# Kernel optimization log

Hardware: AMD Instinct MI355X
Metric: run time of the kernel (lower is better)

Reference implementation:

```python
import jax, jax.numpy as jnp
import numpy as np

B, T, Y, X, E, TR, R = 64, 1024, 512, 128, 512, 512, 512


def setup_inputs() -> dict:
    key = jax.random.key(0)
    ks = iter(jax.random.split(key, 48))

    def w(shape, s=0.05):
        return (jax.random.normal(next(ks), shape, jnp.float32) * s)

    z = lambda *s: jnp.zeros(s, jnp.float32)
    inp = dict(
        data=jax.random.uniform(next(ks), (B, T, Y), jnp.float32),
        eps_q=jax.random.normal(next(ks), (T, B, X), jnp.float32),
        eps_p=jax.random.normal(next(ks), (T, B, X), jnp.float32),
        # RNN (single layer, relu nonlinearity)
        rnn_Wih=w((Y, R)), rnn_Whh=w((R, R)), rnn_bih=z(R), rnn_bhh=z(R),
        h0=z(R), xq0=z(X), x0=z(X),
        # GaussianCombiner
        comb_Wxh=w((X, R)), comb_bxh=z(R),
        comb_Whm=w((R, X)), comb_bhm=z(X),
        comb_Whl=w((R, X)), comb_bhl=z(X),
        # GaussianGatedTransition
        t_Wg1=w((X, TR)), t_bg1=z(TR), t_Wg2=w((TR, X)), t_bg2=z(X),
        t_Wp1=w((X, TR)), t_bp1=z(TR), t_Wp2=w((TR, X)), t_bp2=z(X),
        t_Wmu=jnp.eye(X, dtype=jnp.float32), t_bmu=z(X),  # torch inits lin_x_to_mu to identity
        t_Wlv=w((X, X)), t_blv=z(X),
        # BernoulliEmitter
        e_W1=w((X, E)), e_b1=z(E), e_W2=w((E, E)), e_b2=z(E),
        e_W3=w((E, Y)), e_b3=z(Y),
    )
    return inp


def reference(data, eps_q, eps_p,
              rnn_Wih, rnn_Whh, rnn_bih, rnn_bhh, h0, xq0, x0,
              comb_Wxh, comb_bxh, comb_Whm, comb_bhm, comb_Whl, comb_bhl,
              t_Wg1, t_bg1, t_Wg2, t_bg2, t_Wp1, t_bp1, t_Wp2, t_bp2,
              t_Wmu, t_bmu, t_Wlv, t_blv,
              e_W1, e_b1, e_W2, e_b2, e_W3, e_b3):
    Bx = data.shape[0]

    # ---- inference RNN: run on time-reversed data, then reverse output back ----
    # precompute input projection for all steps: [T, B, R]
    x_proj = (jnp.einsum('bty,yr->btr', data[:, ::-1, :], rnn_Wih)
              + rnn_bih + rnn_bhh).transpose(1, 0, 2)

    def rnn_step(h, xp):
        h = jax.nn.relu(xp + h @ rnn_Whh)
        return h, h

    h_init = jnp.broadcast_to(h0, (Bx, R))
    _, hs = jax.lax.scan(rnn_step, h_init, x_proj)  # [T, B, R]
    rnn_out = hs[::-1]  # back to original time order, aligned with data

    # ---- inference network: sequential combiner + reparameterize ----
    def inf_step(x_prev, inputs):
        h_rnn, eps = inputs
        h_c = 0.5 * (jnp.tanh(x_prev @ comb_Wxh + comb_bxh) + h_rnn)
        mu = h_c @ comb_Whm + comb_bhm
        lv = h_c @ comb_Whl + comb_bhl
        x_t = mu + eps * jnp.exp(0.5 * lv)
        return x_t, (x_t, mu, lv)

    xq0b = jnp.broadcast_to(xq0, (Bx, X))
    _, (q_x, q_mu, q_lv) = jax.lax.scan(inf_step, xq0b, (rnn_out, eps_q))
    q_x, q_mu, q_lv = (a.transpose(1, 0, 2) for a in (q_x, q_mu, q_lv))  # [B,T,X]

    # ---- generative model: sequential gated transition ----
    def gen_step(x_prev, eps):
        gate = jax.nn.sigmoid(jax.nn.relu(x_prev @ t_Wg1 + t_bg1) @ t_Wg2 + t_bg2)
        pm = jax.nn.relu(x_prev @ t_Wp1 + t_bp1) @ t_Wp2 + t_bp2
        mu = (1.0 - gate) * (x_prev @ t_Wmu + t_bmu) + gate * pm
        lv = jax.nn.relu(pm) @ t_Wlv + t_blv
        x_t = mu + eps * jnp.exp(0.5 * lv)
        return x_t, (x_t, mu, lv)

    x0b = jnp.broadcast_to(x0, (Bx, X))
    _, (p_x, p_mu, p_lv) = jax.lax.scan(gen_step, x0b, eps_p)
    p_x, p_mu, p_lv = (a.transpose(1, 0, 2) for a in (p_x, p_mu, p_lv))  # [B,T,X]

    # ---- emitter over all (b, t) at once ----
    h1 = jax.nn.relu(jnp.einsum('btx,xe->bte', q_x, e_W1) + e_b1)
    h2 = jax.nn.relu(jnp.einsum('bte,ef->btf', h1, e_W2) + e_b2)
    y_probs = jax.nn.sigmoid(jnp.einsum('bte,ey->bty', h2, e_W3) + e_b3)

    return (q_x, q_mu, q_lv, p_x, p_mu, p_lv, y_probs)
```

## Files before the change

kernel.cpp:

```cpp
#include <hip/hip_runtime.h>
#include <stdint.h>

typedef __bf16 bf16x8 __attribute__((ext_vector_type(8)));
typedef short  s16x8  __attribute__((ext_vector_type(8)));
typedef float  f32x4  __attribute__((ext_vector_type(4)));

#define MFMA16(a, b, c) __builtin_amdgcn_mfma_f32_16x16x32_bf16((a), (b), (c), 0, 0, 0)

#define OFF_X      0ull
#define OFF_QXBF   67108864ull
#define OFF_WIH    83886080ull
#define OFF_WHH    84410368ull
#define OFF_WXH    84934656ull
#define OFF_WICAT  85065728ull
#define OFF_W1CAT  85327872ull
#define OFF_WG2    85590016ull
#define OFF_WP2    85721088ull
#define OFF_WMU    85852160ull
#define OFF_WLV    85884928ull
#define OFF_EW1    85917696ull
#define OFF_EW2    86048768ull
#define OFF_EW3    86573056ull
#define OFF_B1CAT  87097344ull
#define OFF_BICAT  87101440ull
#define OFF_XPCNT  87364608ull

#define QX_O  0ull
#define QMU_O 8388608ull
#define QLV_O 16777216ull
#define PX_O  25165824ull
#define PMU_O 33554432ull
#define PLV_O 41943040ull
#define Y_O   50331648ull

#define SMEM_SCAN 131072
#define SMEM_EMIS 133120

struct P {
  char* ws; float* out;
  const float *data, *eps_q, *eps_p;
  const float *Wih, *Whh, *bih, *bhh, *h0, *xq0, *x0;
  const float *Wxh, *bxh, *Whm, *bhm, *Whl, *bhl;
  const float *Wg1, *bg1, *Wg2, *bg2, *Wp1, *bp1, *Wp2, *bp2, *Wmu, *bmu, *Wlv, *blv;
  const float *eW1, *eb1, *eW2, *eb2, *eW3, *eb3;
};

__device__ __forceinline__ short f2bf(float f) {
  union { float f; uint32_t u; } v; v.f = f;
  uint32_t r = (v.u + 0x7FFFu + ((v.u >> 16) & 1u)) >> 16;
  return (short)(uint16_t)r;
}
__device__ __forceinline__ float bf2f(short s) {
  union { uint32_t u; float f; } v; v.u = ((uint32_t)(uint16_t)s) << 16;
  return v.f;
}
__device__ __forceinline__ bf16x8 ldfrag(const short* pp) { return *(const bf16x8*)pp; }
__device__ __forceinline__ bf16x8 cvt8p(const float* pp) {
  bf16x8 r;
#pragma unroll
  for (int i = 0; i < 8; ++i) r[i] = (__bf16)pp[i];
  return r;
}
__device__ __forceinline__ bf16x8 relu8(bf16x8 a) {
  s16x8 s = __builtin_bit_cast(s16x8, a);
#pragma unroll
  for (int i = 0; i < 8; ++i) s[i] = (s[i] < 0) ? (short)0 : s[i];
  return __builtin_bit_cast(bf16x8, s);
}

__device__ __forceinline__ void relfence() {
  asm volatile("s_waitcnt vmcnt(0)" ::: "memory");
}
__device__ __forceinline__ void st_sc16(short* pp, short v) {
  __hip_atomic_store(pp, v, __ATOMIC_RELAXED, __HIP_MEMORY_SCOPE_AGENT);
}
__device__ __forceinline__ short ld_sc16(const short* pp) {
  return __hip_atomic_load((short*)pp, __ATOMIC_RELAXED, __HIP_MEMORY_SCOPE_AGENT);
}
__device__ __forceinline__ int ldflag(int* pp) {
  return __hip_atomic_load(pp, __ATOMIC_RELAXED, __HIP_MEMORY_SCOPE_AGENT);
}
__device__ __forceinline__ void barrier_lgkm() {
  __builtin_amdgcn_sched_barrier(0);
  asm volatile("s_waitcnt lgkmcnt(0)" ::: "memory");
  __builtin_amdgcn_s_barrier();
  __builtin_amdgcn_sched_barrier(0);
}

__device__ __forceinline__ void pack_w(short* dst, const float* src, int KT, int N, int idx) {
  int tile = idx >> 9, rem = idx & 511;
  int lane = rem >> 3, j = rem & 7;
  int nt = tile / KT, kt = tile - nt * KT;
  int k = kt * 32 + ((lane >> 4) << 3) + j, n = (nt << 4) + (lane & 15);
  dst[idx] = f2bf(src[(int64_t)k * N + n]);
}

__global__ void __launch_bounds__(256) k_prep(P p) {
  char* ws = p.ws;
  const int64_t total = 1608032;
  for (int64_t i = (int64_t)blockIdx.x * 256 + threadIdx.x; i < total;
       i += (int64_t)gridDim.x * 256) {
    int64_t r = i;
    if (r < 262144) { pack_w((short*)(ws + OFF_WIH), p.Wih, 16, 512, (int)r); continue; }
    r -= 262144;
    if (r < 262144) { pack_w((short*)(ws + OFF_WHH), p.Whh, 16, 512, (int)r); continue; }
    r -= 262144;
    if (r < 65536) { pack_w((short*)(ws + OFF_WXH), p.Wxh, 4, 512, (int)r); continue; }
    r -= 65536;
    if (r < 131072) {
      int idx = (int)r;
      int tile = idx >> 9, rem = idx & 511, lane = rem >> 3, jj = rem & 7;
      int nt = tile >> 4, kt = tile & 15;
      int k = kt * 32 + ((lane >> 4) << 3) + jj, ccol = (nt << 4) + (lane & 15);
      int pair = ccol >> 7, within = ccol & 127, sub = within >> 6;
      int col = (within & 63) + (pair << 6);
      const float* s = sub ? p.Whl : p.Whm;
      ((short*)(ws + OFF_WICAT))[idx] = f2bf(s[(int64_t)k * 128 + col]);
      continue;
    }
    r -= 131072;
    if (r < 131072) {
      int idx = (int)r;
      int tile = idx >> 9, rem = idx & 511, lane = rem >> 3, jj = rem & 7;
      int nt = tile >> 2, kt = tile & 3;
      int k = kt * 32 + ((lane >> 4) << 3) + jj, ccol = (nt << 4) + (lane & 15);
      const float* s = (ccol < 512) ? p.Wg1 : p.Wp1;
      ((short*)(ws + OFF_W1CAT))[idx] = f2bf(s[(int64_t)k * 512 + (ccol & 511)]);
      continue;
    }
    r -= 131072;
    if (r < 65536) { pack_w((short*)(ws + OFF_WG2), p.Wg2, 16, 128, (int)r); continue; }
    r -= 65536;
    if (r < 65536) { pack_w((short*)(ws + OFF_WP2), p.Wp2, 16, 128, (int)r); continue; }
    r -= 65536;
    if (r < 16384) { pack_w((short*)(ws + OFF_WMU), p.Wmu, 4, 128, (int)r); continue; }
    r -= 16384;
    if (r < 16384) { pack_w((short*)(ws + OFF_WLV), p.Wlv, 4, 128, (int)r); continue; }
    r -= 16384;
    if (r < 65536) { pack_w((short*)(ws + OFF_EW1), p.eW1, 4, 512, (int)r); continue; }
    r -= 65536;
    if (r < 262144) { pack_w((short*)(ws + OFF_EW2), p.eW2, 16, 512, (int)r); continue; }
    r -= 262144;
    if (r < 262144) { pack_w((short*)(ws + OFF_EW3), p.eW3, 16, 512, (int)r); continue; }
    r -= 262144;
    if (r < 1024) { ((float*)(ws + OFF_B1CAT))[r] = (r < 512) ? p.bg1[r] : p.bp1[r - 512]; continue; }
    r -= 1024;
    if (r < 256) {
      int ccol = (int)r; int pair = ccol >> 7, within = ccol & 127, sub = within >> 6;
      int col = (within & 63) + (pair << 6);
      ((float*)(ws + OFF_BICAT))[ccol] = sub ? p.bhl[col] : p.bhm[col];
      continue;
    }
    r -= 256;
    ((int*)(ws + OFF_XPCNT))[r] = 0;
  }
}

__global__ void __launch_bounds__(512, 2) k_scan(P p) {
  extern __shared__ char smem[];
  char* ws = p.ws;
  const int tid = threadIdx.x;
  const int lane = tid & 63, w = tid >> 6;
  const int l16 = lane & 15, quad = lane >> 4;
  const int wg = blockIdx.x;

  short* Xb   = (short*)(ws + OFF_X);
  short* qxbf = (short*)(ws + OFF_QXBF);
  int* xp_cnt = (int*)(ws + OFF_XPCNT);

  if (wg < 64) {
    const int s = wg & 7, t0 = wg >> 3;
    const int mrow4 = (w & 3) * 16;
    const int nt0 = s * 4 + (w >> 2) * 2;
    const short* wih = (const short*)(ws + OFF_WIH);
    for (int tt = 0; tt < 128; ++tt) {
      const int t = t0 + (tt << 3);
      const int tsrc = 1023 - t;
      const float* arow = p.data + ((size_t)(mrow4 + l16) * 1024 + tsrc) * 512 + quad * 8;
      f32x4 acc[2] = {};
      for (int kt = 0; kt < 16; ++kt) {
        bf16x8 af = cvt8p(arow + kt * 32);
#pragma unroll
        for (int i = 0; i < 2; ++i) {
          bf16x8 bw = ldfrag(wih + ((size_t)((nt0 + i) * 16 + kt) * 64 + lane) * 8);
          acc[i] = MFMA16(af, bw, acc[i]);
        }
      }
      short* xrow = Xb + (size_t)t * 32768;
#pragma unroll
      for (int i = 0; i < 2; ++i) {
        const int col = (nt0 + i) * 16 + l16;
        const float bias = p.bih[col] + p.bhh[col];
#pragma unroll
        for (int r = 0; r < 4; ++r) {
          const int row = mrow4 + quad * 4 + r;
          st_sc16(xrow + (size_t)row * 512 + col, f2bf(acc[i][r] + bias));
        }
      }
      relfence();
      __syncthreads();
      if (tid == 0) atomicAdd(xp_cnt + t, 1);
    }
    return;
  }

  if (wg < 68) {
    const int g = wg - 64;
    short* whh_l = (short*)smem;
    char* hbuf = smem + 98304;
    {
      const float4* src4 = (const float4*)(ws + OFF_WHH);
      float4* dst4 = (float4*)smem;
      for (int i2 = tid; i2 < 6144; i2 += 512) {
        const int blk = i2 >> 6, wi = i2 & 63;
        const int nt = blk / 3, kk = blk - nt * 3;
        dst4[(size_t)blk * 64 + wi] = src4[(size_t)(nt * 16 + 13 + kk) * 64 + wi];
      }
    }
    const short* whh = (const short*)(ws + OFF_WHH);
    bf16x8 wb[4][13];
#pragma unroll
    for (int i = 0; i < 4; ++i) {
      const int nt = w * 4 + i;
#pragma unroll
      for (int kt = 0; kt < 13; ++kt)
        wb[i][kt] = ldfrag(whh + ((size_t)(nt * 16 + kt) * 64 + lane) * 8);
    }
    __syncthreads();
    while (ldflag(xp_cnt) < 8) __builtin_amdgcn_s_sleep(2);
    short xv[4][4];
#pragma unroll
    for (int i = 0; i < 4; ++i) {
      const int col = (w * 4 + i) * 16 + l16;
#pragma unroll
      for (int r = 0; r < 4; ++r)
        xv[i][r] = ld_sc16(Xb + (size_t)(g * 16 + quad * 4 + r) * 512 + col);
    }
    {
      f32x4 acc[4] = {};
#pragma unroll
      for (int c = 0; c < 8; ++c) {
        bf16x8 a2[2];
#pragma unroll
        for (int k2 = 0; k2 < 2; ++k2) a2[k2] = cvt8p(p.h0 + (c * 2 + k2) * 32 + quad * 8);
#pragma unroll
        for (int k2 = 0; k2 < 2; ++k2) {
          const int kt = c * 2 + k2;
#pragma unroll
          for (int i = 0; i < 4; ++i) {
            bf16x8 bw = (kt < 13)
                ? wb[i][kt]
                : ldfrag(whh_l + ((size_t)((w * 4 + i) * 3 + (kt - 13)) * 64 + lane) * 8);
            acc[i] = MFMA16(a2[k2], bw, acc[i]);
          }
        }
      }
      char* hw = hbuf;
      short* xrow = Xb;
#pragma unroll
      for (int i = 0; i < 4; ++i) {
        const int col = (w * 4 + i) * 16 + l16;
#pragma unroll
        for (int r = 0; r < 4; ++r) {
          const int row = quad * 4 + r;
          float h = acc[i][r] + bf2f(xv[i][r]);
          const short hv = f2bf(h > 0.f ? h : 0.f);
          *(short*)(hw + row * 1024 + ((col * 2) ^ ((row & 7) << 4))) = hv;
          st_sc16(xrow + (size_t)(g * 16 + row) * 512 + col, hv);
        }
      }
      while (ldflag(xp_cnt + 1) < 8) __builtin_amdgcn_s_sleep(2);
      const short* xn = Xb + 32768;
#pragma unroll
      for (int i = 0; i < 4; ++i) {
        const int col = (w * 4 + i) * 16 + l16;
#pragma unroll
        for (int r = 0; r < 4; ++r)
          xv[i][r] = ld_sc16(xn + (size_t)(g * 16 + quad * 4 + r) * 512 + col);
      }
      barrier_lgkm();
    }
    for (int t = 1; t < 1024; ++t) {
      const char* hb = hbuf + ((t - 1) & 1) * 16384;
      f32x4 acc[4] = {};
#pragma unroll
      for (int c = 0; c < 8; ++c) {
        bf16x8 a2[2];
#pragma unroll
        for (int k2 = 0; k2 < 2; ++k2) {
          const int kt = c * 2 + k2;
          a2[k2] = ldfrag((const short*)(hb + l16 * 1024 +
                     ((kt * 64 + quad * 16) ^ ((l16 & 7) << 4))));
        }
#pragma unroll
        for (int k2 = 0; k2 < 2; ++k2) {
          const int kt = c * 2 + k2;
#pragma unroll
          for (int i = 0; i < 4; ++i) {
            bf16x8 bw = (kt < 13)
                ? wb[i][kt]
                : ldfrag(whh_l + ((size_t)((w * 4 + i) * 3 + (kt - 13)) * 64 + lane) * 8);
            acc[i] = MFMA16(a2[k2], bw, acc[i]);
          }
        }
      }
      char* hw = hbuf + (t & 1) * 16384;
      short* xrow = Xb + (size_t)t * 32768;
#pragma unroll
      for (int i = 0; i < 4; ++i) {
        const int col = (w * 4 + i) * 16 + l16;
#pragma unroll
        for (int r = 0; r < 4; ++r) {
          const int row = quad * 4 + r;
          float h = acc[i][r] + bf2f(xv[i][r]);
          const short hv = f2bf(h > 0.f ? h : 0.f);
          *(short*)(hw + row * 1024 + ((col * 2) ^ ((row & 7) << 4))) = hv;
          st_sc16(xrow + (size_t)(g * 16 + row) * 512 + col, hv);
        }
      }
      if (t < 1023) {
        int* fc = xp_cnt + t + 1;
        while (ldflag(fc) < 8) __builtin_amdgcn_s_sleep(2);
        const short* xn = Xb + (size_t)(t + 1) * 32768;
#pragma unroll
        for (int i = 0; i < 4; ++i) {
          const int col = (w * 4 + i) * 16 + l16;
#pragma unroll
          for (int r = 0; r < 4; ++r)
            xv[i][r] = ld_sc16(xn + (size_t)(g * 16 + quad * 4 + r) * 512 + col);
        }
      }
      barrier_lgkm();
    }
    relfence();
    __syncthreads();
    const int g2 = g;
    char* hcs = smem;
    char* xqs = smem + 16384;
    float* scr = (float*)(smem + 20480);
    const short* wxh = (const short*)(ws + OFF_WXH);
    const short* wicat = (const short*)(ws + OFF_WICAT);
    const float* bicat = (const float*)(ws + OFF_BICAT);
    bf16x8 wa[4][4];
    float bx[4];
#pragma unroll
    for (int i = 0; i < 4; ++i) {
      const int nt = w * 4 + i;
#pragma unroll
      for (int kt = 0; kt < 4; ++kt)
        wa[i][kt] = ldfrag(wxh + ((size_t)(nt * 4 + kt) * 64 + lane) * 8);
      bx[i] = p.bxh[nt * 16 + l16];
    }
    bf16x8 wbv[2][16];
    float bias2[2];
#pragma unroll
    for (int i = 0; i < 2; ++i) {
      const int nt = w * 2 + i;
#pragma unroll
      for (int kt = 0; kt < 16; ++kt)
        wbv[i][kt] = ldfrag(wicat + ((size_t)(nt * 16 + kt) * 64 + lane) * 8);
      bias2[i] = bicat[nt * 16 + l16];
    }
    for (int t = 0; t < 1024; ++t) {
      short rv[4][4];
      const short* rsrc = Xb + (size_t)(1023 - t) * 32768;
#pragma unroll
      for (int i = 0; i < 4; ++i) {
        const int ng = (w * 4 + i) * 16 + l16;
#pragma unroll
        for (int r = 0; r < 4; ++r)
          rv[i][r] = ld_sc16(rsrc + (size_t)(g2 * 16 + quad * 4 + r) * 512 + ng);
      }
      float ev[4];
#pragma unroll
      for (int q2 = 0; q2 < 4; ++q2) {
        const int idx = tid + q2 * 512;
        const int row = idx >> 7, cl = idx & 127;
        ev[q2] = p.eps_q[((size_t)t * 64 + g2 * 16 + row) * 128 + cl];
      }
      bf16x8 af1[4];
      if (t == 0) {
#pragma unroll
        for (int kt = 0; kt < 4; ++kt) af1[kt] = cvt8p(p.xq0 + kt * 32 + quad * 8);
      } else {
#pragma unroll
        for (int kt = 0; kt < 4; ++kt)
          af1[kt] = ldfrag((const short*)(xqs + l16 * 256 +
                     ((kt * 64 + quad * 16) ^ ((l16 & 7) << 4))));
      }
      f32x4 acc1[4] = {};
#pragma unroll
      for (int kt = 0; kt < 4; ++kt)
#pragma unroll
        for (int i = 0; i < 4; ++i) acc1[i] = MFMA16(af1[kt], wa[i][kt], acc1[i]);
#pragma unroll
      for (int i = 0; i < 4; ++i) {
        const int ng = (w * 4 + i) * 16 + l16;
#pragma unroll
        for (int r = 0; r < 4; ++r) {
          const int row = quad * 4 + r;
          const float u = acc1[i][r] + bx[i];
          const float e = __expf(2.f * u);
          const float th = 1.f - 2.f / (e + 1.f);
          const float hcv = 0.5f * (th + bf2f(rv[i][r]));
          *(short*)(hcs + row * 1024 + ((ng * 2) ^ ((row & 7) << 4))) = f2bf(hcv);
        }
      }
      barrier_lgkm();
      f32x4 acc2[2] = {};
#pragma unroll
      for (int c = 0; c < 4; ++c) {
        bf16x8 a4[4];
#pragma unroll
        for (int k2 = 0; k2 < 4; ++k2) {
          const int kt = c * 4 + k2;
          a4[k2] = ldfrag((const short*)(hcs + l16 * 1024 +
                     ((kt * 64 + quad * 16) ^ ((l16 & 7) << 4))));
        }
#pragma unroll
        for (int k2 = 0; k2 < 4; ++k2)
#pragma unroll
          for (int i = 0; i < 2; ++i) acc2[i] = MFMA16(a4[k2], wbv[i][c * 4 + k2], acc2[i]);
      }
#pragma unroll
      for (int i = 0; i < 2; ++i) {
        const int catcol = (w * 2 + i) * 16 + l16;
        const int within = catcol & 127, sub = within >> 6;
        const int col = (within & 63) + ((catcol >> 7) << 6);
        float* dbase = p.out + (sub ? QLV_O : QMU_O);
#pragma unroll
        for (int r = 0; r < 4; ++r) {
          const int row = quad * 4 + r;
          const float v = acc2[i][r] + bias2[i];
          dbase[(size_t)(g2 * 16 + row) * 131072 + (size_t)t * 128 + col] = v;
          scr[(sub * 16 + row) * 128 + col] = v;
        }
      }
      barrier_lgkm();
#pragma unroll
      for (int q2 = 0; q2 < 4; ++q2) {
        const int idx = tid + q2 * 512;
        const int row = idx >> 7, cl = idx & 127;
        const int b = g2 * 16 + row;
        const float m = scr[row * 128 + cl], l = scr[(16 + row) * 128 + cl];
        const float xvv = m + ev[q2] * __expf(0.5f * l);
        p.out[QX_O + (size_t)b * 131072 + (size_t)t * 128 + cl] = xvv;
        const short xb = f2bf(xvv);
        qxbf[((size_t)b * 1024 + t) * 128 + cl] = xb;
        *(short*)(xqs + row * 256 + ((cl * 2) ^ ((row & 7) << 4))) = xb;
      }
      barrier_lgkm();
    }
    return;
  }

  {
    const int g3 = wg - 68;
    short* ldsWmu = (short*)smem;
    short* ldsWlv = (short*)(smem + 32768);
    char* xls  = smem + 65536;
    char* u1ls = smem + 69632;
    char* pmls = smem + 102400;
    {
      const float4* s1 = (const float4*)(ws + OFF_WMU);
      const float4* s2 = (const float4*)(ws + OFF_WLV);
      float4* d1 = (float4*)smem;
      float4* d2 = (float4*)(smem + 32768);
      for (int i2 = tid; i2 < 2048; i2 += 512) { d1[i2] = s1[i2]; d2[i2] = s2[i2]; }
    }
    const short* w1cat = (const short*)(ws + OFF_W1CAT);
    const float* b1cat = (const float*)(ws + OFF_B1CAT);
    const short* wp2g = (const short*)(ws + OFF_WP2);
    const short* wg2g = (const short*)(ws + OFF_WG2);
    bf16x8 w1[8][4];
    float b1[8];
#pragma unroll
    for (int i = 0; i < 8; ++i) {
      const int nt = w * 8 + i;
#pragma unroll
      for (int kt = 0; kt < 4; ++kt)
        w1[i][kt] = ldfrag(w1cat + ((size_t)(nt * 4 + kt) * 64 + lane) * 8);
      b1[i] = b1cat[nt * 16 + l16];
    }
    const int colw = w * 16 + l16;
    const float bpv = p.bp2[colw], bgv = p.bg2[colw], bmv = p.bmu[colw], blvv = p.blv[colw];
    __syncthreads();
    for (int t = 0; t < 1024; ++t) {
      float ep[4];
#pragma unroll
      for (int r = 0; r < 4; ++r)
        ep[r] = p.eps_p[((size_t)t * 64 + g3 * 16 + quad * 4 + r) * 128 + colw];
      bf16x8 ax[4];
      if (t == 0) {
#pragma unroll
        for (int kt = 0; kt < 4; ++kt) ax[kt] = cvt8p(p.x0 + kt * 32 + quad * 8);
      } else {
#pragma unroll
        for (int kt = 0; kt < 4; ++kt)
          ax[kt] = ldfrag((const short*)(xls + l16 * 256 +
                     ((kt * 64 + quad * 16) ^ ((l16 & 7) << 4))));
      }
#pragma unroll
      for (int hf = 0; hf < 2; ++hf) {
        f32x4 a1[4] = {};
#pragma unroll
        for (int kt = 0; kt < 4; ++kt)
#pragma unroll
          for (int i = 0; i < 4; ++i) a1[i] = MFMA16(ax[kt], w1[hf * 4 + i][kt], a1[i]);
#pragma unroll
        for (int i = 0; i < 4; ++i) {
          const int c1 = (w * 8 + hf * 4 + i) * 16 + l16;
#pragma unroll
          for (int r = 0; r < 4; ++r) {
            const int row = quad * 4 + r;
            const float u = a1[i][r] + b1[hf * 4 + i];
            *(short*)(u1ls + row * 2048 + ((c1 * 2) ^ ((row & 7) << 4))) = f2bf(u > 0.f ? u : 0.f);
          }
        }
      }
      barrier_lgkm();
      f32x4 apm = {}, ag = {}, axm = {};
#pragma unroll
      for (int c = 0; c < 8; ++c) {
        bf16x8 bpf[2], bgf[2];
#pragma unroll
        for (int k2 = 0; k2 < 2; ++k2) {
          bpf[k2] = ldfrag(wp2g + ((size_t)(w * 16 + c * 2 + k2) * 64 + lane) * 8);
          bgf[k2] = ldfrag(wg2g + ((size_t)(w * 16 + c * 2 + k2) * 64 + lane) * 8);
        }
        bf16x8 aup[2], aug[2];
#pragma unroll
        for (int k2 = 0; k2 < 2; ++k2) {
          const int kt = c * 2 + k2;
          aup[k2] = ldfrag((const short*)(u1ls + l16 * 2048 +
                      ((1024 + kt * 64 + quad * 16) ^ ((l16 & 7) << 4))));
          aug[k2] = ldfrag((const short*)(u1ls + l16 * 2048 +
                      ((kt * 64 + quad * 16) ^ ((l16 & 7) << 4))));
        }
#pragma unroll
        for (int k2 = 0; k2 < 2; ++k2) {
          apm = MFMA16(aup[k2], bpf[k2], apm);
          ag  = MFMA16(aug[k2], bgf[k2], ag);
        }
      }
#pragma unroll
      for (int kt = 0; kt < 4; ++kt) {
        bf16x8 bw = ldfrag(ldsWmu + ((size_t)(w * 4 + kt) * 64 + lane) * 8);
        axm = MFMA16(ax[kt], bw, axm);
      }
      float pmv[4];
#pragma unroll
      for (int r = 0; r < 4; ++r) {
        const int row = quad * 4 + r;
        pmv[r] = apm[r] + bpv;
        *(short*)(pmls + row * 256 + ((colw * 2) ^ ((row & 7) << 4))) = f2bf(pmv[r]);
      }
      barrier_lgkm();
      bf16x8 apf[4];
#pragma unroll
      for (int kt = 0; kt < 4; ++kt)
        apf[kt] = relu8(ldfrag((const short*)(pmls + l16 * 256 +
                    ((kt * 64 + quad * 16) ^ ((l16 & 7) << 4)))));
      f32x4 alv = {};
#pragma unroll
      for (int kt = 0; kt < 4; ++kt) {
        bf16x8 bw = ldfrag(ldsWlv + ((size_t)(w * 4 + kt) * 64 + lane) * 8);
        alv = MFMA16(apf[kt], bw, alv);
      }
#pragma unroll
      for (int r = 0; r < 4; ++r) {
        const int row = quad * 4 + r, b = g3 * 16 + row;
        const float lv = alv[r] + blvv;
        const float gv = 1.f / (1.f + __expf(-(ag[r] + bgv)));
        const float xmv = axm[r] + bmv;
        const float mu = (1.f - gv) * xmv + gv * pmv[r];
        const float xvv = mu + ep[r] * __expf(0.5f * lv);
        *(short*)(xls + row * 256 + ((colw * 2) ^ ((row & 7) << 4))) = f2bf(xvv);
        p.out[PMU_O + (size_t)b * 131072 + (size_t)t * 128 + colw] = mu;
        p.out[PLV_O + (size_t)b * 131072 + (size_t)t * 128 + colw] = lv;
        p.out[PX_O  + (size_t)b * 131072 + (size_t)t * 128 + colw] = xvv;
      }
      barrier_lgkm();
    }
    return;
  }
}

__global__ void __launch_bounds__(256) k_emis(P p) {
  extern __shared__ char smem[];
  short* h1 = (short*)smem;
  short* h2 = (short*)(smem + 66560);
  const int tid = threadIdx.x, lane = tid & 63, w = tid >> 6;
  const int l16 = lane & 15, quad = lane >> 4;
  const size_t m0 = (size_t)blockIdx.x * 64;
  const short* qx  = (const short*)(p.ws + OFF_QXBF);
  const short* ew1 = (const short*)(p.ws + OFF_EW1);
  const short* ew2 = (const short*)(p.ws + OFF_EW2);
  const short* ew3 = (const short*)(p.ws + OFF_EW3);
  for (int nc = 0; nc < 2; ++nc) {
    f32x4 acc[4][4] = {};
    for (int kt = 0; kt < 4; ++kt) {
      bf16x8 bw[4];
#pragma unroll
      for (int i = 0; i < 4; ++i) {
        const int nt = w * 8 + nc * 4 + i;
        bw[i] = ldfrag(ew1 + ((size_t)(nt * 4 + kt) * 64 + lane) * 8);
      }
#pragma unroll
      for (int mt = 0; mt < 4; ++mt) {
        bf16x8 af = ldfrag(qx + (m0 + mt * 16 + l16) * 128 + kt * 32 + quad * 8);
#pragma unroll
        for (int i = 0; i < 4; ++i) acc[mt][i] = MFMA16(af, bw[i], acc[mt][i]);
      }
    }
#pragma unroll
    for (int mt = 0; mt < 4; ++mt)
#pragma unroll
      for (int i = 0; i < 4; ++i) {
        const int col = (w * 8 + nc * 4 + i) * 16 + l16;
        const float bias = p.eb1[col];
#pragma unroll
        for (int r = 0; r < 4; ++r) {
          const float v = acc[mt][i][r] + bias;
          h1[(mt * 16 + quad * 4 + r) * 520 + col] = f2bf(v > 0.f ? v : 0.f);
        }
      }
  }
  __syncthreads();
  for (int nc = 0; nc < 2; ++nc) {
    f32x4 acc[4][4] = {};
    for (int kt = 0; kt < 16; ++kt) {
      bf16x8 bw[4];
#pragma unroll
      for (int i = 0; i < 4; ++i) {
        const int nt = w * 8 + nc * 4 + i;
        bw[i] = ldfrag(ew2 + ((size_t)(nt * 16 + kt) * 64 + lane) * 8);
      }
#pragma unroll
      for (int mt = 0; mt < 4; ++mt) {
        bf16x8 af = ldfrag(h1 + (mt * 16 + l16) * 520 + kt * 32 + quad * 8);
#pragma unroll
        for (int i = 0; i < 4; ++i) acc[mt][i] = MFMA16(af, bw[i], acc[mt][i]);
      }
    }
#pragma unroll
    for (int mt = 0; mt < 4; ++mt)
#pragma unroll
      for (int i = 0; i < 4; ++i) {
        const int col = (w * 8 + nc * 4 + i) * 16 + l16;
        const float bias = p.eb2[col];
#pragma unroll
        for (int r = 0; r < 4; ++r) {
          const float v = acc[mt][i][r] + bias;
          h2[(mt * 16 + quad * 4 + r) * 520 + col] = f2bf(v > 0.f ? v : 0.f);
        }
      }
  }
  __syncthreads();
  for (int nc = 0; nc < 2; ++nc) {
    f32x4 acc[4][4] = {};
    for (int kt = 0; kt < 16; ++kt) {
      bf16x8 bw[4];
#pragma unroll
      for (int i = 0; i < 4; ++i) {
        const int nt = w * 8 + nc * 4 + i;
        bw[i] = ldfrag(ew3 + ((size_t)(nt * 16 + kt) * 64 + lane) * 8);
      }
#pragma unroll
      for (int mt = 0; mt < 4; ++mt) {
        bf16x8 af = ldfrag(h2 + (mt * 16 + l16) * 520 + kt * 32 + quad * 8);
#pragma unroll
        for (int i = 0; i < 4; ++i) acc[mt][i] = MFMA16(af, bw[i], acc[mt][i]);
      }
    }
#pragma unroll
    for (int mt = 0; mt < 4; ++mt)
#pragma unroll
      for (int i = 0; i < 4; ++i) {
        const int col = (w * 8 + nc * 4 + i) * 16 + l16;
        const float bias = p.eb3[col];
#pragma unroll
        for (int r = 0; r < 4; ++r) {
          const size_t m = m0 + mt * 16 + quad * 4 + r;
          const size_t b = m >> 10, tt2 = m & 1023;
          const float v = acc[mt][i][r] + bias;
          p.out[Y_O + (b << 19) + tt2 * 512 + col] = 1.f / (1.f + __expf(-v));
        }
      }
  }
}

extern "C" void kernel_launch(void* const* d_in, const int* in_sizes, int n_in,
                              void* d_out, int out_size, void* d_ws, size_t ws_size,
                              hipStream_t stream) {
  (void)in_sizes; (void)n_in; (void)out_size; (void)ws_size;
  P p;
  p.ws = (char*)d_ws; p.out = (float*)d_out;
  p.data = (const float*)d_in[0];
  p.eps_q = (const float*)d_in[1];
  p.eps_p = (const float*)d_in[2];
  p.Wih = (const float*)d_in[3]; p.Whh = (const float*)d_in[4];
  p.bih = (const float*)d_in[5]; p.bhh = (const float*)d_in[6];
  p.h0 = (const float*)d_in[7]; p.xq0 = (const float*)d_in[8]; p.x0 = (const float*)d_in[9];
  p.Wxh = (const float*)d_in[10]; p.bxh = (const float*)d_in[11];
  p.Whm = (const float*)d_in[12]; p.bhm = (const float*)d_in[13];
  p.Whl = (const float*)d_in[14]; p.bhl = (const float*)d_in[15];
  p.Wg1 = (const float*)d_in[16]; p.bg1 = (const float*)d_in[17];
  p.Wg2 = (const float*)d_in[18]; p.bg2 = (const float*)d_in[19];
  p.Wp1 = (const float*)d_in[20]; p.bp1 = (const float*)d_in[21];
  p.Wp2 = (const float*)d_in[22]; p.bp2 = (const float*)d_in[23];
  p.Wmu = (const float*)d_in[24]; p.bmu = (const float*)d_in[25];
  p.Wlv = (const float*)d_in[26]; p.blv = (const float*)d_in[27];
  p.eW1 = (const float*)d_in[28]; p.eb1 = (const float*)d_in[29];
  p.eW2 = (const float*)d_in[30]; p.eb2 = (const float*)d_in[31];
  p.eW3 = (const float*)d_in[32]; p.eb3 = (const float*)d_in[33];

  hipFuncSetAttribute(reinterpret_cast<const void*>(k_scan),
                      hipFuncAttributeMaxDynamicSharedMemorySize, SMEM_SCAN);
  hipFuncSetAttribute(reinterpret_cast<const void*>(k_emis),
                      hipFuncAttributeMaxDynamicSharedMemorySize, SMEM_EMIS);

  k_prep<<<dim3(2048), dim3(256), 0, stream>>>(p);
  k_scan<<<dim3(72), dim3(512), SMEM_SCAN, stream>>>(p);
  k_emis<<<dim3(1024), dim3(256), SMEM_EMIS, stream>>>(p);
}
```

Measured before the change: 12.99 ms.

## Split input projection into its own kernel and drop per-step flag polling

The input projection (data @ Wih) moves out of the persistent scan kernel into a separate 512-block kernel that runs before the scan. The scan grid shrinks from 72 to 8 workgroups. This removes the per-timestep counter flags, the spin-wait polling and the agent-scope atomic 16-bit loads and stores on the RNN critical path; plain loads and stores replace them. In exchange, the projection no longer overlaps with the recurrence and adds a serialized launch. Any remaining cross-workgroup handoff of RNN outputs now uses plain loads, which may rely on coherence guarantees the code does not enforce.

```diff
diff --git a/kernel.cpp b/kernel.cpp
--- a/kernel.cpp
+++ b/kernel.cpp
@@ -23,7 +23,6 @@
 #define OFF_EW3    86573056ull
 #define OFF_B1CAT  87097344ull
 #define OFF_BICAT  87101440ull
-#define OFF_XPCNT  87364608ull
 
 #define QX_O  0ull
 #define QMU_O 8388608ull
@@ -67,18 +66,8 @@
   for (int i = 0; i < 8; ++i) s[i] = (s[i] < 0) ? (short)0 : s[i];
   return __builtin_bit_cast(bf16x8, s);
 }
-
 __device__ __forceinline__ void relfence() {
   asm volatile("s_waitcnt vmcnt(0)" ::: "memory");
-}
-__device__ __forceinline__ void st_sc16(short* pp, short v) {
-  __hip_atomic_store(pp, v, __ATOMIC_RELAXED, __HIP_MEMORY_SCOPE_AGENT);
-}
-__device__ __forceinline__ short ld_sc16(const short* pp) {
-  return __hip_atomic_load((short*)pp, __ATOMIC_RELAXED, __HIP_MEMORY_SCOPE_AGENT);
-}
-__device__ __forceinline__ int ldflag(int* pp) {
-  return __hip_atomic_load(pp, __ATOMIC_RELAXED, __HIP_MEMORY_SCOPE_AGENT);
 }
 __device__ __forceinline__ void barrier_lgkm() {
   __builtin_amdgcn_sched_barrier(0);
@@ -97,7 +86,7 @@
 
 __global__ void __launch_bounds__(256) k_prep(P p) {
   char* ws = p.ws;
-  const int64_t total = 1608032;
+  const int64_t total = 1606912;
   for (int64_t i = (int64_t)blockIdx.x * 256 + threadIdx.x; i < total;
        i += (int64_t)gridDim.x * 256) {
     int64_t r = i;
@@ -151,12 +140,47 @@
       ((float*)(ws + OFF_BICAT))[ccol] = sub ? p.bhl[col] : p.bhm[col];
       continue;
     }
-    r -= 256;
-    ((int*)(ws + OFF_XPCNT))[r] = 0;
   }
 }
 
-__global__ void __launch_bounds__(512, 2) k_scan(P p) {
+__global__ void __launch_bounds__(256) k_xproj(P p) {
+  char* ws = p.ws;
+  const int tid = threadIdx.x;
+  const int lane = tid & 63, w = tid >> 6;
+  const int l16 = lane & 15, quad = lane >> 4;
+  const int s = blockIdx.x & 7, t0 = blockIdx.x >> 3;
+  short* Xb = (short*)(ws + OFF_X);
+  const short* wih = (const short*)(ws + OFF_WIH);
+  for (int tt = 0; tt < 16; ++tt) {
+    const int t = t0 + (tt << 6);
+    const int tsrc = 1023 - t;
+    const float* arow = p.data + ((size_t)(w * 16 + l16) * 1024 + tsrc) * 512 + quad * 8;
+    f32x4 acc[4] = {};
+    for (int kt = 0; kt < 16; ++kt) {
+      bf16x8 af = cvt8p(arow + kt * 32);
+#pragma unroll
+      for (int i = 0; i < 4; ++i) {
+        const int nt = s * 4 + i;
+        bf16x8 bw = ldfrag(wih + ((size_t)(nt * 16 + kt) * 64 + lane) * 8);
+        acc[i] = MFMA16(af, bw, acc[i]);
+      }
+    }
+    short* xrow = Xb + (size_t)t * 32768;
+#pragma unroll
+    for (int i = 0; i < 4; ++i) {
+      const int col = (s * 4 + i) * 16 + l16;
+      const float bias = p.bih[col] + p.bhh[col];
+#pragma unroll
+      for (int r = 0; r < 4; ++r) {
+        const int row = w * 16 + quad * 4 + r;
+        xrow[(size_t)row * 512 + col] = f2bf(acc[i][r] + bias);
+      }
+    }
+  }
+}
+
+__global__ void __launch_bounds__(512)
+__attribute__((amdgpu_waves_per_eu(2, 2))) k_scan(P p) {
   extern __shared__ char smem[];
   char* ws = p.ws;
   const int tid = threadIdx.x;
@@ -166,46 +190,9 @@
 
   short* Xb   = (short*)(ws + OFF_X);
   short* qxbf = (short*)(ws + OFF_QXBF);
-  int* xp_cnt = (int*)(ws + OFF_XPCNT);
-
-  if (wg < 64) {
-    const int s = wg & 7, t0 = wg >> 3;
-    const int mrow4 = (w & 3) * 16;
-    const int nt0 = s * 4 + (w >> 2) * 2;
-    const short* wih = (const short*)(ws + OFF_WIH);
-    for (int tt = 0; tt < 128; ++tt) {
-      const int t = t0 + (tt << 3);
-      const int tsrc = 1023 - t;
-      const float* arow = p.data + ((size_t)(mrow4 + l16) * 1024 + tsrc) * 512 + quad * 8;
-      f32x4 acc[2] = {};
-      for (int kt = 0; kt < 16; ++kt) {
-        bf16x8 af = cvt8p(arow + kt * 32);
-#pragma unroll
-        for (int i = 0; i < 2; ++i) {
-          bf16x8 bw = ldfrag(wih + ((size_t)((nt0 + i) * 16 + kt) * 64 + lane) * 8);
-          acc[i] = MFMA16(af, bw, acc[i]);
-        }
-      }
-      short* xrow = Xb + (size_t)t * 32768;
-#pragma unroll
-      for (int i = 0; i < 2; ++i) {
-        const int col = (nt0 + i) * 16 + l16;
-        const float bias = p.bih[col] + p.bhh[col];
-#pragma unroll
-        for (int r = 0; r < 4; ++r) {
-          const int row = mrow4 + quad * 4 + r;
-          st_sc16(xrow + (size_t)row * 512 + col, f2bf(acc[i][r] + bias));
-        }
-      }
-      relfence();
-      __syncthreads();
-      if (tid == 0) atomicAdd(xp_cnt + t, 1);
-    }
-    return;
-  }
-
-  if (wg < 68) {
-    const int g = wg - 64;
+
+  if (wg < 4) {
+    const int g = wg;
     short* whh_l = (short*)smem;
     char* hbuf = smem + 98304;
     {
@@ -227,14 +214,13 @@
         wb[i][kt] = ldfrag(whh + ((size_t)(nt * 16 + kt) * 64 + lane) * 8);
     }
     __syncthreads();
-    while (ldflag(xp_cnt) < 8) __builtin_amdgcn_s_sleep(2);
     short xv[4][4];
 #pragma unroll
     for (int i = 0; i < 4; ++i) {
       const int col = (w * 4 + i) * 16 + l16;
 #pragma unroll
       for (int r = 0; r < 4; ++r)
-        xv[i][r] = ld_sc16(Xb + (size_t)(g * 16 + quad * 4 + r) * 512 + col);
+        xv[i][r] = Xb[(size_t)(g * 16 + quad * 4 + r) * 512 + col];
     }
     {
       f32x4 acc[4] = {};
@@ -256,7 +242,6 @@
         }
       }
       char* hw = hbuf;
-      short* xrow = Xb;
 #pragma unroll
       for (int i = 0; i < 4; ++i) {
         const int col = (w * 4 + i) * 16 + l16;
@@ -266,17 +251,16 @@
           float h = acc[i][r] + bf2f(xv[i][r]);
           const short hv = f2bf(h > 0.f ? h : 0.f);
           *(short*)(hw + row * 1024 + ((col * 2) ^ ((row & 7) << 4))) = hv;
-          st_sc16(xrow + (size_t)(g * 16 + row) * 512 + col, hv);
-        }
-      }
-      while (ldflag(xp_cnt + 1) < 8) __builtin_amdgcn_s_sleep(2);
+          Xb[(size_t)(g * 16 + row) * 512 + col] = hv;
+        }
+      }
       const short* xn = Xb + 32768;
 #pragma unroll
       for (int i = 0; i < 4; ++i) {
         const int col = (w * 4 + i) * 16 + l16;
 #pragma unroll
         for (int r = 0; r < 4; ++r)
-          xv[i][r] = ld_sc16(xn + (size_t)(g * 16 + quad * 4 + r) * 512 + col);
+          xv[i][r] = xn[(size_t)(g * 16 + quad * 4 + r) * 512 + col];
       }
       barrier_lgkm();
     }
@@ -315,19 +299,17 @@
           float h = acc[i][r] + bf2f(xv[i][r]);
           const short hv = f2bf(h > 0.f ? h : 0.f);
           *(short*)(hw + row * 1024 + ((col * 2) ^ ((row & 7) << 4))) = hv;
-          st_sc16(xrow + (size_t)(g * 16 + row) * 512 + col, hv);
+          xrow[(size_t)(g * 16 + row) * 512 + col] = hv;
         }
       }
       if (t < 1023) {
-        int* fc = xp_cnt + t + 1;
-        while (ldflag(fc) < 8) __builtin_amdgcn_s_sleep(2);
         const short* xn = Xb + (size_t)(t + 1) * 32768;
 #pragma unroll
         for (int i = 0; i < 4; ++i) {
           const int col = (w * 4 + i) * 16 + l16;
 #pragma unroll
           for (int r = 0; r < 4; ++r)
-            xv[i][r] = ld_sc16(xn + (size_t)(g * 16 + quad * 4 + r) * 512 + col);
+            xv[i][r] = xn[(size_t)(g * 16 + quad * 4 + r) * 512 + col];
         }
       }
       barrier_lgkm();
@@ -369,7 +351,7 @@
         const int ng = (w * 4 + i) * 16 + l16;
 #pragma unroll
         for (int r = 0; r < 4; ++r)
-          rv[i][r] = ld_sc16(rsrc + (size_t)(g2 * 16 + quad * 4 + r) * 512 + ng);
+          rv[i][r] = rsrc[(size_t)(g2 * 16 + quad * 4 + r) * 512 + ng];
       }
       float ev[4];
 #pragma unroll
@@ -455,7 +437,7 @@
   }
 
   {
-    const int g3 = wg - 68;
+    const int g3 = wg - 4;
     short* ldsWmu = (short*)smem;
     short* ldsWlv = (short*)(smem + 32768);
     char* xls  = smem + 65536;
@@ -721,6 +703,7 @@
                       hipFuncAttributeMaxDynamicSharedMemorySize, SMEM_EMIS);
 
   k_prep<<<dim3(2048), dim3(256), 0, stream>>>(p);
-  k_scan<<<dim3(72), dim3(512), SMEM_SCAN, stream>>>(p);
+  k_xproj<<<dim3(512), dim3(256), 0, stream>>>(p);
+  k_scan<<<dim3(8), dim3(512), SMEM_SCAN, stream>>>(p);
   k_emis<<<dim3(1024), dim3(256), SMEM_EMIS, stream>>>(p);
 }
```

After: 11.99 ms. 7.7% less time.
